# Kernel tuning notes

Measured on AMD Instinct MI355X. Metric: run time of the kernel, lower is better.

## Reference

```python
import jax, jax.numpy as jnp
import numpy as np

N_ATOMS = 500_000
N_PAIRS = 16_000_000
A0 = 0.5291772105638411
KE = 14.399645351950548
KEHALF = KE / 2.0


def softplus_inverse(x):
    # inverse of softplus: log(exp(x) - 1)
    return float(np.log(np.expm1(x)))


def setup_inputs() -> dict:
    key = jax.random.key(0)
    k_z, k_r, k_c, k_i, k_j = jax.random.split(key, 5)
    Zf = jax.random.randint(k_z, (N_ATOMS,), 1, 95).astype(jnp.float32)
    rij = jax.random.uniform(k_r, (N_PAIRS,), minval=0.5, maxval=5.0, dtype=jnp.float32)
    cutoff_values = jax.random.uniform(k_c, (N_PAIRS,), dtype=jnp.float32)
    idx_i = jax.random.randint(k_i, (N_PAIRS,), 0, N_ATOMS)
    idx_j = jax.random.randint(k_j, (N_PAIRS,), 0, N_ATOMS)
    p = lambda v: jnp.full((1,), softplus_inverse(v), dtype=jnp.float32)
    return {
        "N": N_ATOMS,
        "Zf": Zf,
        "rij": rij,
        "cutoff_values": cutoff_values,
        "idx_i": idx_i,
        "idx_j": idx_j,
        "adiv": p(1.0 / (0.8854 * A0)),
        "apow": p(0.23),
        "c1": p(0.1818),
        "c2": p(0.5099),
        "c3": p(0.2802),
        "c4": p(0.02817),
        "a1": p(3.2),
        "a2": p(0.9423),
        "a3": p(0.4028),
        "a4": p(0.2016),
    }


def reference(N, Zf, rij, cutoff_values, idx_i, idx_j,
              adiv, apow, c1, c2, c3, c4, a1, a2, a3, a4):
    sp = jax.nn.softplus
    # per-atom screened charge: [N]
    z = Zf ** sp(apow)
    # per-pair screening length: [P]
    a = (z[idx_i] + z[idx_j]) * sp(adiv)
    a1p = sp(a1) * a
    a2p = sp(a2) * a
    a3p = sp(a3) * a
    a4p = sp(a4) * a
    c1p, c2p, c3p, c4p = sp(c1), sp(c2), sp(c3), sp(c4)
    csum = c1p + c2p + c3p + c4p
    c1n, c2n, c3n, c4n = c1p / csum, c2p / csum, c3p / csum, c4p / csum
    zizj = Zf[idx_i] * Zf[idx_j]
    f = (c1n * jnp.exp(-a1p * rij)
         + c2n * jnp.exp(-a2p * rij)
         + c3n * jnp.exp(-a3p * rij)
         + c4n * jnp.exp(-a4p * rij)) * cutoff_values
    contrib = KEHALF * f * zizj / rij  # [P]
    return jnp.zeros((N,), dtype=Zf.dtype).at[idx_i].add(contrib)
```

## Files before the change

kernel.cpp:

```cpp
#include <hip/hip_runtime.h>
#include <hip/hip_fp16.h>

static constexpr float KEHALF = 7.199822675975274f;
static constexpr int APB = 2048;
static constexpr int APB_SHIFT = 11;
static constexpr int NBMAX = 256;
static constexpr int CHUNK = 8192;
static constexpr int ABLK = 512;
static constexpr int BBLK = 1024;
static constexpr int CTILE = 2048;

typedef float v4f __attribute__((ext_vector_type(4)));
typedef int   v4i __attribute__((ext_vector_type(4)));
typedef unsigned v4u __attribute__((ext_vector_type(4)));

__global__ void zbl_tables_kernel(const float* __restrict__ adiv,
                                  const float* __restrict__ apow,
                                  const float* __restrict__ c1,
                                  const float* __restrict__ c2,
                                  const float* __restrict__ c3,
                                  const float* __restrict__ c4,
                                  const float* __restrict__ a1,
                                  const float* __restrict__ a2,
                                  const float* __restrict__ a3,
                                  const float* __restrict__ a4,
                                  float* __restrict__ consts,
                                  float* __restrict__ lutA) {
    __shared__ float sA[2];
    int t = threadIdx.x;
    if (t == 0) {
        auto sp = [](float x) { return log1pf(expf(x)); };
        float c1p = sp(*c1), c2p = sp(*c2), c3p = sp(*c3), c4p = sp(*c4);
        float inv = 1.0f / (c1p + c2p + c3p + c4p);
        consts[0] = sp(*apow);
        consts[1] = sp(*adiv);
        consts[2] = c1p * inv; consts[3] = c2p * inv;
        consts[4] = c3p * inv; consts[5] = c4p * inv;
        consts[6] = sp(*a1); consts[7] = sp(*a2);
        consts[8] = sp(*a3); consts[9] = sp(*a4);
        sA[0] = consts[0]; sA[1] = consts[1];
    }
    __syncthreads();
    if (t < 96)
        lutA[t] = (t == 0) ? 0.0f : sA[1] * expf(sA[0] * logf((float)t));
}

__global__ void zbl_pack_kernel(const float* __restrict__ Zf,
                                unsigned char* __restrict__ zb, int N) {
    int i = blockIdx.x * blockDim.x + threadIdx.x;
    if (i < N) zb[i] = (unsigned char)(Zf[i] + 0.5f);
}

__global__ void __launch_bounds__(ABLK)
zbl_phaseA(const int* __restrict__ idx_i, const int* __restrict__ idx_j,
           const float* __restrict__ rij, const float* __restrict__ cut,
           const unsigned char* __restrict__ zb,
           const float* __restrict__ consts, const float* __restrict__ lutA,
           unsigned* __restrict__ recs, unsigned short* __restrict__ starts,
           int P, int NB) {
    __shared__ unsigned hist[NBMAX];
    __shared__ unsigned scanv[NBMAX];
    __shared__ unsigned cursor[NBMAX];
    __shared__ float lA[96];
    __shared__ unsigned stage[CHUNK];

    const int t = threadIdx.x;
    const int c = blockIdx.x;
    const int base = c * CHUNK;
    const int lim = min(base + CHUNK, P);
    const int cnt = lim - base;
    const int n4 = cnt >> 2;

    for (int b = t; b < NBMAX; b += ABLK) hist[b] = 0;
    if (t < 96) lA[t] = lutA[t];
    __syncthreads();

    {
        const v4i* ii4 = reinterpret_cast<const v4i*>(idx_i + base);
        for (int q = t; q < n4; q += ABLK) {
            v4i ii = __builtin_nontemporal_load(ii4 + q);
            atomicAdd(&hist[(unsigned)ii[0] >> APB_SHIFT], 1u);
            atomicAdd(&hist[(unsigned)ii[1] >> APB_SHIFT], 1u);
            atomicAdd(&hist[(unsigned)ii[2] >> APB_SHIFT], 1u);
            atomicAdd(&hist[(unsigned)ii[3] >> APB_SHIFT], 1u);
        }
        for (int p = n4 * 4 + t; p < cnt; p += ABLK)
            atomicAdd(&hist[(unsigned)idx_i[base + p] >> APB_SHIFT], 1u);
    }
    __syncthreads();

    if (t < NBMAX) scanv[t] = hist[t];
    __syncthreads();
    for (int off = 1; off < NBMAX; off <<= 1) {
        unsigned v = 0;
        if (t < NBMAX && t >= off) v = scanv[t - off];
        __syncthreads();
        if (t < NBMAX && t >= off) scanv[t] += v;
        __syncthreads();
    }
    if (t < NBMAX) cursor[t] = scanv[t] - hist[t];
    {
        const int S = NB + 1;
        for (int b = t; b <= NB; b += ABLK)
            starts[(size_t)c * S + b] =
                (unsigned short)(b == 0 ? 0u : scanv[b - 1]);
    }
    __syncthreads();

    const float c1n = consts[2], c2n = consts[3], c3n = consts[4], c4n = consts[5];
    const float a1 = consts[6], a2 = consts[7], a3 = consts[8], a4 = consts[9];

    auto process = [&](int i, int j, float r, float cu) {
        unsigned bi = zb[i], bj = zb[j];
        float aij = lA[bi] + lA[bj];
        float ar = aij * r;
        float f = c1n * __expf(-a1 * ar) + c2n * __expf(-a2 * ar)
                + c3n * __expf(-a3 * ar) + c4n * __expf(-a4 * ar);
        float contrib = KEHALF * f * cu * (float)bi * (float)bj *
                        __builtin_amdgcn_rcpf(r);
        unsigned b = (unsigned)i >> APB_SHIFT;
        unsigned rank = atomicAdd(&cursor[b], 1u);
        stage[rank] = (((unsigned)i & (APB - 1)) << 16)
                    | (unsigned)__half_as_ushort(__float2half_rn(contrib));
    };

    {
        const v4i* ii4 = reinterpret_cast<const v4i*>(idx_i + base);
        const v4i* jj4 = reinterpret_cast<const v4i*>(idx_j + base);
        const v4f* rr4 = reinterpret_cast<const v4f*>(rij + base);
        const v4f* cc4 = reinterpret_cast<const v4f*>(cut + base);
        for (int q = t; q < n4; q += ABLK) {
            v4i ii = __builtin_nontemporal_load(ii4 + q);
            v4i jj = __builtin_nontemporal_load(jj4 + q);
            v4f rr = __builtin_nontemporal_load(rr4 + q);
            v4f cc = __builtin_nontemporal_load(cc4 + q);
#pragma unroll
            for (int k = 0; k < 4; ++k) process(ii[k], jj[k], rr[k], cc[k]);
        }
        for (int p = n4 * 4 + t; p < cnt; p += ABLK)
            process(idx_i[base + p], idx_j[base + p], rij[base + p], cut[base + p]);
    }
    __syncthreads();

    {
        const v4u* src = reinterpret_cast<const v4u*>(stage);
        v4u* dst = reinterpret_cast<v4u*>(recs + (size_t)base);
        for (int k = t; k < CHUNK / 4; k += ABLK)
            __builtin_nontemporal_store(src[k], dst + k);
    }
}

__global__ void __launch_bounds__(BBLK)
zbl_phaseB(const unsigned* __restrict__ recs,
           const unsigned short* __restrict__ starts,
           float* __restrict__ out, int N, int NB, int nchunks) {
    __shared__ float acc[APB];
    __shared__ unsigned short s0s[CTILE];
    __shared__ unsigned short s1s[CTILE];
    const int t = threadIdx.x;
    const int b = blockIdx.x;
    const int S = NB + 1;
    for (int i = t; i < APB; i += BBLK) acc[i] = 0.f;

    const int wave = t >> 6, lane = t & 63, nw = BBLK / 64;

    for (int cb = 0; cb < nchunks; cb += CTILE) {
        const int ce = min(cb + CTILE, nchunks);
        __syncthreads();
        for (int c = cb + t; c < ce; c += BBLK) {
            s0s[c - cb] = starts[(size_t)c * S + b];
            s1s[c - cb] = starts[(size_t)c * S + b + 1];
        }
        __syncthreads();
        for (int c = cb + wave; c < ce; c += nw) {
            unsigned s0 = s0s[c - cb], s1 = s1s[c - cb];
            const unsigned* seg = recs + (size_t)c * CHUNK;
            for (unsigned u = s0 + lane; u < s1; u += 64) {
                unsigned rec = __builtin_nontemporal_load(seg + u);
                float v = __half2float(__ushort_as_half((unsigned short)(rec & 0xffffu)));
                atomicAdd(&acc[rec >> 16], v);
            }
        }
    }
    __syncthreads();

    const int abase = b << APB_SHIFT;
    for (int i = t; i < APB; i += BBLK) {
        int g = abase + i;
        if (g < N) out[g] = acc[i];
    }
}

__global__ void __launch_bounds__(256)
zbl_pair_fallback(const v4f* __restrict__ rij4, const v4f* __restrict__ cut4,
                  const v4i* __restrict__ ii4, const v4i* __restrict__ jj4,
                  const float* __restrict__ Zf, const float* __restrict__ consts,
                  float* __restrict__ out, int P4) {
    int t = blockIdx.x * blockDim.x + threadIdx.x;
    if (t >= P4) return;
    const float sp_apow = consts[0], sp_adiv = consts[1];
    const float c1n = consts[2], c2n = consts[3], c3n = consts[4], c4n = consts[5];
    const float a1 = consts[6], a2 = consts[7], a3 = consts[8], a4 = consts[9];
    v4f rr = rij4[t]; v4f cc = cut4[t]; v4i ii = ii4[t]; v4i jj = jj4[t];
#pragma unroll
    for (int k = 0; k < 4; ++k) {
        int i = ii[k], j = jj[k];
        float zfi = Zf[i], zfj = Zf[j];
        float zi = __expf(sp_apow * __logf(zfi));
        float zj = __expf(sp_apow * __logf(zfj));
        float a = (zi + zj) * sp_adiv;
        float ar = a * rr[k];
        float f = c1n * __expf(-a1 * ar) + c2n * __expf(-a2 * ar)
                + c3n * __expf(-a3 * ar) + c4n * __expf(-a4 * ar);
        atomicAdd(&out[i],
                  KEHALF * f * cc[k] * zfi * zfj * __builtin_amdgcn_rcpf(rr[k]));
    }
}

extern "C" void kernel_launch(void* const* d_in, const int* in_sizes, int n_in,
                              void* d_out, int out_size, void* d_ws, size_t ws_size,
                              hipStream_t stream) {
    const float* Zf = (const float*)d_in[1];
    const float* rij = (const float*)d_in[2];
    const float* cut = (const float*)d_in[3];
    const int* idx_i = (const int*)d_in[4];
    const int* idx_j = (const int*)d_in[5];
    const int N = in_sizes[1];
    const int P = in_sizes[2];
    float* out = (float*)d_out;

    const int NB = (N + APB - 1) / APB;
    const int nchunks = (P + CHUNK - 1) / CHUNK;

    size_t recs_bytes = (size_t)nchunks * CHUNK * 4;
    size_t starts_bytes = (size_t)nchunks * (NB + 1) * 2;
    size_t consts_off = (recs_bytes + starts_bytes + 255) & ~(size_t)255;
    size_t lut_off = consts_off + 16 * 4;
    size_t zb_off = lut_off + 96 * 4;
    size_t need = zb_off + (size_t)N + 64;

    if (NB <= NBMAX && ws_size >= need) {
        unsigned* recs = (unsigned*)d_ws;
        unsigned short* starts = (unsigned short*)((char*)d_ws + recs_bytes);
        float* consts = (float*)((char*)d_ws + consts_off);
        float* lutA = (float*)((char*)d_ws + lut_off);
        unsigned char* zb = (unsigned char*)((char*)d_ws + zb_off);

        zbl_tables_kernel<<<1, 128, 0, stream>>>(
            (const float*)d_in[6], (const float*)d_in[7],
            (const float*)d_in[8], (const float*)d_in[9],
            (const float*)d_in[10], (const float*)d_in[11],
            (const float*)d_in[12], (const float*)d_in[13],
            (const float*)d_in[14], (const float*)d_in[15], consts, lutA);

        zbl_pack_kernel<<<(N + 255) / 256, 256, 0, stream>>>(Zf, zb, N);

        zbl_phaseA<<<nchunks, ABLK, 0, stream>>>(
            idx_i, idx_j, rij, cut, zb, consts, lutA, recs, starts, P, NB);

        zbl_phaseB<<<NB, BBLK, 0, stream>>>(recs, starts, out, N, NB, nchunks);
    } else {
        float* consts = (float*)d_ws;
        float* lutA = consts + 16;
        hipMemsetAsync(out, 0, (size_t)out_size * sizeof(float), stream);
        zbl_tables_kernel<<<1, 128, 0, stream>>>(
            (const float*)d_in[6], (const float*)d_in[7],
            (const float*)d_in[8], (const float*)d_in[9],
            (const float*)d_in[10], (const float*)d_in[11],
            (const float*)d_in[12], (const float*)d_in[13],
            (const float*)d_in[14], (const float*)d_in[15], consts, lutA);
        zbl_pair_fallback<<<(P / 4 + 255) / 256, 256, 0, stream>>>(
            (const v4f*)rij, (const v4f*)cut, (const v4i*)idx_i,
            (const v4i*)idx_j, Zf, consts, out, P / 4);
    }
}
```

Measured before the change: 488.2 us.

## Replace two-phase binned scatter with single fused kernel using global atomics

Removes the table, pack, binning phase A and accumulation phase B kernels and replaces them with one grid-stride kernel. Each block computes the softplus constants and the per-Z screening LUT itself, gathers Zf directly, and atomically adds each pair's contribution into the output. This drops the workspace record traffic, several launches and the fp16 quantization of contributions. In exchange it relies on 16M random global float atomics, which may contend and cost more than the sorted shared-memory accumulation. It also needs a memset of the output.

```diff
diff --git a/kernel.cpp b/kernel.cpp
--- a/kernel.cpp
+++ b/kernel.cpp
@@ -1,219 +1,80 @@
 #include <hip/hip_runtime.h>
-#include <hip/hip_fp16.h>
 
 static constexpr float KEHALF = 7.199822675975274f;
-static constexpr int APB = 2048;
-static constexpr int APB_SHIFT = 11;
-static constexpr int NBMAX = 256;
-static constexpr int CHUNK = 8192;
-static constexpr int ABLK = 512;
-static constexpr int BBLK = 1024;
-static constexpr int CTILE = 2048;
 
 typedef float v4f __attribute__((ext_vector_type(4)));
 typedef int   v4i __attribute__((ext_vector_type(4)));
-typedef unsigned v4u __attribute__((ext_vector_type(4)));
 
-__global__ void zbl_tables_kernel(const float* __restrict__ adiv,
-                                  const float* __restrict__ apow,
-                                  const float* __restrict__ c1,
-                                  const float* __restrict__ c2,
-                                  const float* __restrict__ c3,
-                                  const float* __restrict__ c4,
-                                  const float* __restrict__ a1,
-                                  const float* __restrict__ a2,
-                                  const float* __restrict__ a3,
-                                  const float* __restrict__ a4,
-                                  float* __restrict__ consts,
-                                  float* __restrict__ lutA) {
-    __shared__ float sA[2];
-    int t = threadIdx.x;
-    if (t == 0) {
-        auto sp = [](float x) { return log1pf(expf(x)); };
-        float c1p = sp(*c1), c2p = sp(*c2), c3p = sp(*c3), c4p = sp(*c4);
-        float inv = 1.0f / (c1p + c2p + c3p + c4p);
-        consts[0] = sp(*apow);
-        consts[1] = sp(*adiv);
-        consts[2] = c1p * inv; consts[3] = c2p * inv;
-        consts[4] = c3p * inv; consts[5] = c4p * inv;
-        consts[6] = sp(*a1); consts[7] = sp(*a2);
-        consts[8] = sp(*a3); consts[9] = sp(*a4);
-        sA[0] = consts[0]; sA[1] = consts[1];
-    }
-    __syncthreads();
-    if (t < 96)
-        lutA[t] = (t == 0) ? 0.0f : sA[1] * expf(sA[0] * logf((float)t));
-}
+__global__ void __launch_bounds__(256)
+zbl_direct(const int* __restrict__ idx_i, const int* __restrict__ idx_j,
+           const float* __restrict__ rij, const float* __restrict__ cut,
+           const float* __restrict__ Zf,
+           const float* __restrict__ adiv, const float* __restrict__ apow,
+           const float* __restrict__ c1, const float* __restrict__ c2,
+           const float* __restrict__ c3, const float* __restrict__ c4,
+           const float* __restrict__ a1p, const float* __restrict__ a2p,
+           const float* __restrict__ a3p, const float* __restrict__ a4p,
+           float* __restrict__ out, int P) {
+    __shared__ float lA[96];
 
-__global__ void zbl_pack_kernel(const float* __restrict__ Zf,
-                                unsigned char* __restrict__ zb, int N) {
-    int i = blockIdx.x * blockDim.x + threadIdx.x;
-    if (i < N) zb[i] = (unsigned char)(Zf[i] + 0.5f);
-}
+    auto sp = [](float x) { return log1pf(expf(x)); };
+    const float c1p = sp(*c1), c2p = sp(*c2), c3p = sp(*c3), c4p = sp(*c4);
+    const float inv = 1.0f / (c1p + c2p + c3p + c4p);
+    const float c1n = c1p * inv, c2n = c2p * inv;
+    const float c3n = c3p * inv, c4n = c4p * inv;
+    const float a1 = sp(*a1p), a2 = sp(*a2p), a3 = sp(*a3p), a4 = sp(*a4p);
+    const float sp_apow = sp(*apow), sp_adiv = sp(*adiv);
 
-__global__ void __launch_bounds__(ABLK)
-zbl_phaseA(const int* __restrict__ idx_i, const int* __restrict__ idx_j,
-           const float* __restrict__ rij, const float* __restrict__ cut,
-           const unsigned char* __restrict__ zb,
-           const float* __restrict__ consts, const float* __restrict__ lutA,
-           unsigned* __restrict__ recs, unsigned short* __restrict__ starts,
-           int P, int NB) {
-    __shared__ unsigned hist[NBMAX];
-    __shared__ unsigned scanv[NBMAX];
-    __shared__ unsigned cursor[NBMAX];
-    __shared__ float lA[96];
-    __shared__ unsigned stage[CHUNK];
-
-    const int t = threadIdx.x;
-    const int c = blockIdx.x;
-    const int base = c * CHUNK;
-    const int lim = min(base + CHUNK, P);
-    const int cnt = lim - base;
-    const int n4 = cnt >> 2;
-
-    for (int b = t; b < NBMAX; b += ABLK) hist[b] = 0;
-    if (t < 96) lA[t] = lutA[t];
+    if (threadIdx.x < 96)
+        lA[threadIdx.x] = (threadIdx.x == 0)
+            ? 0.0f
+            : sp_adiv * __expf(sp_apow * __logf((float)threadIdx.x));
     __syncthreads();
 
-    {
-        const v4i* ii4 = reinterpret_cast<const v4i*>(idx_i + base);
-        for (int q = t; q < n4; q += ABLK) {
-            v4i ii = __builtin_nontemporal_load(ii4 + q);
-            atomicAdd(&hist[(unsigned)ii[0] >> APB_SHIFT], 1u);
-            atomicAdd(&hist[(unsigned)ii[1] >> APB_SHIFT], 1u);
-            atomicAdd(&hist[(unsigned)ii[2] >> APB_SHIFT], 1u);
-            atomicAdd(&hist[(unsigned)ii[3] >> APB_SHIFT], 1u);
+    const int tid = blockIdx.x * 256 + threadIdx.x;
+    const int stride = gridDim.x * 256;
+    const int P4 = P >> 2;
+
+    const v4i* ii4 = reinterpret_cast<const v4i*>(idx_i);
+    const v4i* jj4 = reinterpret_cast<const v4i*>(idx_j);
+    const v4f* rr4 = reinterpret_cast<const v4f*>(rij);
+    const v4f* cc4 = reinterpret_cast<const v4f*>(cut);
+
+    for (int q = tid; q < P4; q += stride) {
+        v4i ii = __builtin_nontemporal_load(ii4 + q);
+        v4i jj = __builtin_nontemporal_load(jj4 + q);
+        v4f rr = __builtin_nontemporal_load(rr4 + q);
+        v4f cc = __builtin_nontemporal_load(cc4 + q);
+
+        float zfi0 = Zf[ii[0]], zfi1 = Zf[ii[1]],
+              zfi2 = Zf[ii[2]], zfi3 = Zf[ii[3]];
+        float zfj0 = Zf[jj[0]], zfj1 = Zf[jj[1]],
+              zfj2 = Zf[jj[2]], zfj3 = Zf[jj[3]];
+
+        auto body = [&](int i, float zfi, float zfj, float r, float cu) {
+            float ar = (lA[(int)zfi] + lA[(int)zfj]) * r;
+            float f = c1n * __expf(-a1 * ar) + c2n * __expf(-a2 * ar)
+                    + c3n * __expf(-a3 * ar) + c4n * __expf(-a4 * ar);
+            atomicAdd(&out[i],
+                      KEHALF * f * cu * zfi * zfj * __builtin_amdgcn_rcpf(r));
+        };
+        body(ii[0], zfi0, zfj0, rr[0], cc[0]);
+        body(ii[1], zfi1, zfj1, rr[1], cc[1]);
+        body(ii[2], zfi2, zfj2, rr[2], cc[2]);
+        body(ii[3], zfi3, zfj3, rr[3], cc[3]);
+    }
+
+    if (tid == 0) {
+        for (int p = P4 << 2; p < P; ++p) {
+            int i = idx_i[p];
+            float zfi = Zf[i], zfj = Zf[idx_j[p]];
+            float r = rij[p];
+            float ar = (lA[(int)zfi] + lA[(int)zfj]) * r;
+            float f = c1n * __expf(-a1 * ar) + c2n * __expf(-a2 * ar)
+                    + c3n * __expf(-a3 * ar) + c4n * __expf(-a4 * ar);
+            atomicAdd(&out[i], KEHALF * f * cut[p] * zfi * zfj *
+                               __builtin_amdgcn_rcpf(r));
         }
-        for (int p = n4 * 4 + t; p < cnt; p += ABLK)
-            atomicAdd(&hist[(unsigned)idx_i[base + p] >> APB_SHIFT], 1u);
-    }
-    __syncthreads();
-
-    if (t < NBMAX) scanv[t] = hist[t];
-    __syncthreads();
-    for (int off = 1; off < NBMAX; off <<= 1) {
-        unsigned v = 0;
-        if (t < NBMAX && t >= off) v = scanv[t - off];
-        __syncthreads();
-        if (t < NBMAX && t >= off) scanv[t] += v;
-        __syncthreads();
-    }
-    if (t < NBMAX) cursor[t] = scanv[t] - hist[t];
-    {
-        const int S = NB + 1;
-        for (int b = t; b <= NB; b += ABLK)
-            starts[(size_t)c * S + b] =
-                (unsigned short)(b == 0 ? 0u : scanv[b - 1]);
-    }
-    __syncthreads();
-
-    const float c1n = consts[2], c2n = consts[3], c3n = consts[4], c4n = consts[5];
-    const float a1 = consts[6], a2 = consts[7], a3 = consts[8], a4 = consts[9];
-
-    auto process = [&](int i, int j, float r, float cu) {
-        unsigned bi = zb[i], bj = zb[j];
-        float aij = lA[bi] + lA[bj];
-        float ar = aij * r;
-        float f = c1n * __expf(-a1 * ar) + c2n * __expf(-a2 * ar)
-                + c3n * __expf(-a3 * ar) + c4n * __expf(-a4 * ar);
-        float contrib = KEHALF * f * cu * (float)bi * (float)bj *
-                        __builtin_amdgcn_rcpf(r);
-        unsigned b = (unsigned)i >> APB_SHIFT;
-        unsigned rank = atomicAdd(&cursor[b], 1u);
-        stage[rank] = (((unsigned)i & (APB - 1)) << 16)
-                    | (unsigned)__half_as_ushort(__float2half_rn(contrib));
-    };
-
-    {
-        const v4i* ii4 = reinterpret_cast<const v4i*>(idx_i + base);
-        const v4i* jj4 = reinterpret_cast<const v4i*>(idx_j + base);
-        const v4f* rr4 = reinterpret_cast<const v4f*>(rij + base);
-        const v4f* cc4 = reinterpret_cast<const v4f*>(cut + base);
-        for (int q = t; q < n4; q += ABLK) {
-            v4i ii = __builtin_nontemporal_load(ii4 + q);
-            v4i jj = __builtin_nontemporal_load(jj4 + q);
-            v4f rr = __builtin_nontemporal_load(rr4 + q);
-            v4f cc = __builtin_nontemporal_load(cc4 + q);
-#pragma unroll
-            for (int k = 0; k < 4; ++k) process(ii[k], jj[k], rr[k], cc[k]);
-        }
-        for (int p = n4 * 4 + t; p < cnt; p += ABLK)
-            process(idx_i[base + p], idx_j[base + p], rij[base + p], cut[base + p]);
-    }
-    __syncthreads();
-
-    {
-        const v4u* src = reinterpret_cast<const v4u*>(stage);
-        v4u* dst = reinterpret_cast<v4u*>(recs + (size_t)base);
-        for (int k = t; k < CHUNK / 4; k += ABLK)
-            __builtin_nontemporal_store(src[k], dst + k);
-    }
-}
-
-__global__ void __launch_bounds__(BBLK)
-zbl_phaseB(const unsigned* __restrict__ recs,
-           const unsigned short* __restrict__ starts,
-           float* __restrict__ out, int N, int NB, int nchunks) {
-    __shared__ float acc[APB];
-    __shared__ unsigned short s0s[CTILE];
-    __shared__ unsigned short s1s[CTILE];
-    const int t = threadIdx.x;
-    const int b = blockIdx.x;
-    const int S = NB + 1;
-    for (int i = t; i < APB; i += BBLK) acc[i] = 0.f;
-
-    const int wave = t >> 6, lane = t & 63, nw = BBLK / 64;
-
-    for (int cb = 0; cb < nchunks; cb += CTILE) {
-        const int ce = min(cb + CTILE, nchunks);
-        __syncthreads();
-        for (int c = cb + t; c < ce; c += BBLK) {
-            s0s[c - cb] = starts[(size_t)c * S + b];
-            s1s[c - cb] = starts[(size_t)c * S + b + 1];
-        }
-        __syncthreads();
-        for (int c = cb + wave; c < ce; c += nw) {
-            unsigned s0 = s0s[c - cb], s1 = s1s[c - cb];
-            const unsigned* seg = recs + (size_t)c * CHUNK;
-            for (unsigned u = s0 + lane; u < s1; u += 64) {
-                unsigned rec = __builtin_nontemporal_load(seg + u);
-                float v = __half2float(__ushort_as_half((unsigned short)(rec & 0xffffu)));
-                atomicAdd(&acc[rec >> 16], v);
-            }
-        }
-    }
-    __syncthreads();
-
-    const int abase = b << APB_SHIFT;
-    for (int i = t; i < APB; i += BBLK) {
-        int g = abase + i;
-        if (g < N) out[g] = acc[i];
-    }
-}
-
-__global__ void __launch_bounds__(256)
-zbl_pair_fallback(const v4f* __restrict__ rij4, const v4f* __restrict__ cut4,
-                  const v4i* __restrict__ ii4, const v4i* __restrict__ jj4,
-                  const float* __restrict__ Zf, const float* __restrict__ consts,
-                  float* __restrict__ out, int P4) {
-    int t = blockIdx.x * blockDim.x + threadIdx.x;
-    if (t >= P4) return;
-    const float sp_apow = consts[0], sp_adiv = consts[1];
-    const float c1n = consts[2], c2n = consts[3], c3n = consts[4], c4n = consts[5];
-    const float a1 = consts[6], a2 = consts[7], a3 = consts[8], a4 = consts[9];
-    v4f rr = rij4[t]; v4f cc = cut4[t]; v4i ii = ii4[t]; v4i jj = jj4[t];
-#pragma unroll
-    for (int k = 0; k < 4; ++k) {
-        int i = ii[k], j = jj[k];
-        float zfi = Zf[i], zfj = Zf[j];
-        float zi = __expf(sp_apow * __logf(zfi));
-        float zj = __expf(sp_apow * __logf(zfj));
-        float a = (zi + zj) * sp_adiv;
-        float ar = a * rr[k];
-        float f = c1n * __expf(-a1 * ar) + c2n * __expf(-a2 * ar)
-                + c3n * __expf(-a3 * ar) + c4n * __expf(-a4 * ar);
-        atomicAdd(&out[i],
-                  KEHALF * f * cc[k] * zfi * zfj * __builtin_amdgcn_rcpf(rr[k]));
     }
 }
 
@@ -225,52 +86,21 @@
     const float* cut = (const float*)d_in[3];
     const int* idx_i = (const int*)d_in[4];
     const int* idx_j = (const int*)d_in[5];
-    const int N = in_sizes[1];
     const int P = in_sizes[2];
     float* out = (float*)d_out;
 
-    const int NB = (N + APB - 1) / APB;
-    const int nchunks = (P + CHUNK - 1) / CHUNK;
+    hipMemsetAsync(out, 0, (size_t)out_size * sizeof(float), stream);
 
-    size_t recs_bytes = (size_t)nchunks * CHUNK * 4;
-    size_t starts_bytes = (size_t)nchunks * (NB + 1) * 2;
-    size_t consts_off = (recs_bytes + starts_bytes + 255) & ~(size_t)255;
-    size_t lut_off = consts_off + 16 * 4;
-    size_t zb_off = lut_off + 96 * 4;
-    size_t need = zb_off + (size_t)N + 64;
+    int nblk = (P / 4 + 255) / 256;
+    if (nblk < 1) nblk = 1;
+    if (nblk > 2048) nblk = 2048;
 
-    if (NB <= NBMAX && ws_size >= need) {
-        unsigned* recs = (unsigned*)d_ws;
-        unsigned short* starts = (unsigned short*)((char*)d_ws + recs_bytes);
-        float* consts = (float*)((char*)d_ws + consts_off);
-        float* lutA = (float*)((char*)d_ws + lut_off);
-        unsigned char* zb = (unsigned char*)((char*)d_ws + zb_off);
-
-        zbl_tables_kernel<<<1, 128, 0, stream>>>(
-            (const float*)d_in[6], (const float*)d_in[7],
-            (const float*)d_in[8], (const float*)d_in[9],
-            (const float*)d_in[10], (const float*)d_in[11],
-            (const float*)d_in[12], (const float*)d_in[13],
-            (const float*)d_in[14], (const float*)d_in[15], consts, lutA);
-
-        zbl_pack_kernel<<<(N + 255) / 256, 256, 0, stream>>>(Zf, zb, N);
-
-        zbl_phaseA<<<nchunks, ABLK, 0, stream>>>(
-            idx_i, idx_j, rij, cut, zb, consts, lutA, recs, starts, P, NB);
-
-        zbl_phaseB<<<NB, BBLK, 0, stream>>>(recs, starts, out, N, NB, nchunks);
-    } else {
-        float* consts = (float*)d_ws;
-        float* lutA = consts + 16;
-        hipMemsetAsync(out, 0, (size_t)out_size * sizeof(float), stream);
-        zbl_tables_kernel<<<1, 128, 0, stream>>>(
-            (const float*)d_in[6], (const float*)d_in[7],
-            (const float*)d_in[8], (const float*)d_in[9],
-            (const float*)d_in[10], (const float*)d_in[11],
-            (const float*)d_in[12], (const float*)d_in[13],
-            (const float*)d_in[14], (const float*)d_in[15], consts, lutA);
-        zbl_pair_fallback<<<(P / 4 + 255) / 256, 256, 0, stream>>>(
-            (const v4f*)rij, (const v4f*)cut, (const v4i*)idx_i,
-            (const v4i*)idx_j, Zf, consts, out, P / 4);
-    }
+    zbl_direct<<<nblk, 256, 0, stream>>>(
+        idx_i, idx_j, rij, cut, Zf,
+        (const float*)d_in[6], (const float*)d_in[7],
+        (const float*)d_in[8], (const float*)d_in[9],
+        (const float*)d_in[10], (const float*)d_in[11],
+        (const float*)d_in[12], (const float*)d_in[13],
+        (const float*)d_in[14], (const float*)d_in[15],
+        out, P);
 }
```

After: 977.2 us. 2x slower.
